# Kernel tuning notes

Measured on AMD Instinct MI355X. Metric: run time of the kernel, lower is better.

## Reference

```python
import jax, jax.numpy as jnp
import numpy as np

D_MODEL = 1024
HEADS = 16
DK = D_MODEL // HEADS
B, S = 2, 2048


def setup_inputs() -> dict:
    key = jax.random.key(0)
    ks = jax.random.split(key, 9)
    s = 0.02
    return {
        "Q": jax.random.normal(ks[0], (B, S, D_MODEL), jnp.float32),
        "K": jax.random.normal(ks[1], (B, S, D_MODEL), jnp.float32),
        "V": jax.random.normal(ks[2], (B, S, D_MODEL), jnp.float32),
        "mask": jnp.ones((B, 1, S), jnp.int32),
        "Wq": jax.random.normal(ks[3], (D_MODEL, D_MODEL), jnp.float32) * s,
        "Wk": jax.random.normal(ks[4], (D_MODEL, D_MODEL), jnp.float32) * s,
        "Wv": jax.random.normal(ks[5], (D_MODEL, D_MODEL), jnp.float32) * s,
        "Wo": jax.random.normal(ks[6], (D_MODEL, D_MODEL), jnp.float32) * s,
        "ln_gamma": jnp.ones((D_MODEL,), jnp.float32),
        "ln_beta": jnp.zeros((D_MODEL,), jnp.float32),
    }


def _layer_norm(x, gamma, beta, eps=1e-5):
    mu = jnp.mean(x, axis=-1, keepdims=True)
    var = jnp.mean(jnp.square(x - mu), axis=-1, keepdims=True)
    return (x - mu) * jax.lax.rsqrt(var + eps) * gamma + beta


def reference(Q, K, V, mask, Wq, Wk, Wv, Wo, ln_gamma, ln_beta):
    # torch Linear(no bias): y = x @ W.T
    def split_heads(x):  # [B,S,D] -> [B,H,S,dk]
        return x.reshape(B, -1, HEADS, DK).transpose(0, 2, 1, 3)

    q = split_heads(Q @ Wq.T)
    k = split_heads(K @ Wk.T)
    v = split_heads(V @ Wv.T)

    # scores: [B,H,Sq,Sk]
    scores = jnp.einsum("bhqd,bhkd->bhqk", q, k) / np.sqrt(DK).astype(np.float32)
    m = mask[:, None, :, :]  # [B,1,1,S] broadcast over heads and queries
    scores = jnp.where(m == 0, -jnp.inf, scores)
    attn = jax.nn.softmax(scores, axis=-1)  # dropout is identity in eval
    out = jnp.einsum("bhqk,bhkd->bhqd", attn, v)
    out = out.transpose(0, 2, 1, 3).reshape(B, -1, D_MODEL)
    out = out @ Wo.T
    return _layer_norm(out + Q, ln_gamma, ln_beta)
```

## Files before the change

kernel.cpp:

```cpp
#include <hip/hip_runtime.h>
#include <hip/hip_bf16.h>
#include <stdint.h>

#define NB 2
#define NS 2048
#define ND 1024
#define NH 16
#define NDK 64
#define NM (NB*NS)

using bf16x8 = __attribute__((ext_vector_type(8))) short;
using f32x4  = __attribute__((ext_vector_type(4))) float;
using f32x16 = __attribute__((ext_vector_type(16))) float;
using u32x4  = __attribute__((ext_vector_type(4))) unsigned;

__device__ __forceinline__ unsigned short f2bf(float f){
  unsigned u = __float_as_uint(f);
  u += 0x7fffu + ((u>>16)&1u);
  return (unsigned short)(u>>16);
}

__device__ __forceinline__ void gload_lds16(const void* g, void* l){
  __builtin_amdgcn_global_load_lds((const __attribute__((address_space(1))) void*)g,
                                   (__attribute__((address_space(3))) void*)l, 16, 0, 0);
}

__device__ __forceinline__ float fexp2(float x){
#if __has_builtin(__builtin_amdgcn_exp2f)
  return __builtin_amdgcn_exp2f(x);
#else
  return __expf(x * 0.69314718056f);
#endif
}

__device__ __forceinline__ unsigned cvtpk_bf16(float lo, float hi){
  unsigned r;
  asm("v_cvt_pk_bf16_f32 %0, %1, %2" : "=v"(r) : "v"(lo), "v"(hi));
  return r;
}

__device__ __forceinline__ void swap32(unsigned &a, unsigned &b){
#if __has_builtin(__builtin_amdgcn_permlane32_swap)
  auto rr = __builtin_amdgcn_permlane32_swap((int)a, (int)b, false, false);
  a = (unsigned)rr[0]; b = (unsigned)rr[1];
#else
  const bool lo = (threadIdx.x & 32) == 0;
  unsigned sa = (unsigned)__shfl_xor((int)a, 32, 64);
  unsigned sb = (unsigned)__shfl_xor((int)b, 32, 64);
  unsigned na = lo ? a : sb;
  unsigned nb = lo ? sa : b;
  a = na; b = nb;
#endif
}

__device__ __forceinline__ f32x16 mfma32(bf16x8 a, bf16x8 b, f32x16 c){
  return __builtin_amdgcn_mfma_f32_32x32x16_bf16(a, b, c, 0, 0, 0);
}

__global__ __launch_bounds__(256) void prep_k(const float* __restrict__ Q, const float* __restrict__ K,
                                              const float* __restrict__ V, const float* __restrict__ Wq,
                                              const float* __restrict__ Wk, const float* __restrict__ Wv,
                                              const float* __restrict__ Wo,
                                              unsigned short* __restrict__ Xbf,
                                              unsigned short* __restrict__ Wbf){
  const int bid = blockIdx.x;
  const float* src; unsigned short* dst; int i;
  if (bid < 12288){
    const int which = bid >> 12;
    src = (which==0) ? Q : (which==1) ? K : V;
    dst = Xbf + ((size_t)which << 22);
    i = (bid & 4095)*256 + threadIdx.x;
  } else {
    const int which = (bid - 12288) >> 10;
    src = (which==0) ? Wq : (which==1) ? Wk : (which==2) ? Wv : Wo;
    dst = Wbf + ((size_t)which << 20);
    i = ((bid - 12288) & 1023)*256 + threadIdx.x;
  }
  float4 v = ((const float4*)src)[i];
  ushort4 o;
  o.x = f2bf(v.x); o.y = f2bf(v.y); o.z = f2bf(v.z); o.w = f2bf(v.w);
  ((ushort4*)dst)[i] = o;
}

__global__ __launch_bounds__(256) void gemm_qkv(const short* __restrict__ Xbf, const short* __restrict__ Wbf,
                                                unsigned short* __restrict__ qh, unsigned short* __restrict__ kh,
                                                unsigned short* __restrict__ vT){
  __shared__ short lsA[2][4096];
  __shared__ short lsB[2][4096];
  const int tid = threadIdx.x;
  const int hw = blockIdx.x;
  const int logical = (hw & 7)*96 + (hw >> 3);
  const int z = logical >> 8, rem = logical & 255;
  const int my = rem >> 3, nx = rem & 7;
  const short* A = Xbf + (size_t)z*NM*ND;
  const short* W = Wbf + (size_t)z*ND*ND;
  unsigned short* out = (z==0) ? qh : (z==1) ? kh : vT;
  const int mode = (z==2) ? 1 : 0;
  const int m0 = my*128, n0 = nx*128;

  const short* gA = A + (size_t)m0*1024;
  const short* gB = W + (size_t)n0*1024;
  const int srow = tid>>2, scol = (tid&3)*8;
  const int w = tid>>6, lane = tid&63, lr = lane&15, lk = lane>>4;
  const int wm = w>>1, wn = w&1;

  f32x4 acc[4][4];
  #pragma unroll
  for (int i=0;i<4;++i)
    #pragma unroll
    for (int j=0;j<4;++j) acc[i][j] = (f32x4){0.f,0.f,0.f,0.f};

  #pragma unroll
  for (int r=0;r<2;++r){
    gload_lds16(gA + (size_t)(r*64+srow)*1024 + scol, &lsA[0][(r*256+tid)*8]);
    gload_lds16(gB + (size_t)(r*64+srow)*1024 + scol, &lsB[0][(r*256+tid)*8]);
  }
  int cur = 0;
  for (int ks=0; ks<32; ++ks){
    __syncthreads();
    if (ks+1 < 32){
      const int k0 = (ks+1)*32;
      #pragma unroll
      for (int r=0;r<2;++r){
        gload_lds16(gA + (size_t)(r*64+srow)*1024 + k0 + scol, &lsA[cur^1][(r*256+tid)*8]);
        gload_lds16(gB + (size_t)(r*64+srow)*1024 + k0 + scol, &lsB[cur^1][(r*256+tid)*8]);
      }
    }
    bf16x8 af[4], bfr[4];
    #pragma unroll
    for (int i=0;i<4;++i){
      af[i]  = *(const bf16x8*)&lsA[cur][(wm*64+i*16+lr)*32 + lk*8];
      bfr[i] = *(const bf16x8*)&lsB[cur][(wn*64+i*16+lr)*32 + lk*8];
    }
    #pragma unroll
    for (int i=0;i<4;++i)
      #pragma unroll
      for (int j=0;j<4;++j)
        acc[i][j] = __builtin_amdgcn_mfma_f32_16x16x32_bf16(af[i], bfr[j], acc[i][j], 0,0,0);
    cur ^= 1;
  }
  #pragma unroll
  for (int i=0;i<4;++i)
    #pragma unroll
    for (int j=0;j<4;++j)
      #pragma unroll
      for (int r=0;r<4;++r){
        const int m = m0 + wm*64 + i*16 + lk*4 + r;
        const int n = n0 + wn*64 + j*16 + lr;
        const float v = acc[i][j][r];
        const int b = m>>11, s = m&2047, h = n>>6, dk = n&63;
        size_t addr;
        if (mode == 0) addr = (((size_t)(b*NH+h))*NS + s)*NDK + dk;
        else           addr = (((size_t)(b*NH+h))*NDK + dk)*NS + s;
        out[addr] = f2bf(v);
      }
}

__global__ __launch_bounds__(256) void gemm_out(const short* __restrict__ Attn, const short* __restrict__ Wo,
                                                const float* __restrict__ Qin, float* __restrict__ proj){
  __shared__ short lsA[2][4096];
  __shared__ short lsB[2][4096];
  const int tid = threadIdx.x;
  const int hw = blockIdx.x;
  const int logical = (hw & 7)*32 + (hw >> 3);
  const int my = logical >> 3, nx = logical & 7;
  const int m0 = my*128, n0 = nx*128;
  const short* gA = Attn + (size_t)m0*1024;
  const short* gB = Wo + (size_t)n0*1024;
  const int srow = tid>>2, scol = (tid&3)*8;
  const int w = tid>>6, lane = tid&63, lr = lane&15, lk = lane>>4;
  const int wm = w>>1, wn = w&1;

  f32x4 acc[4][4];
  #pragma unroll
  for (int i=0;i<4;++i)
    #pragma unroll
    for (int j=0;j<4;++j) acc[i][j] = (f32x4){0.f,0.f,0.f,0.f};

  #pragma unroll
  for (int r=0;r<2;++r){
    gload_lds16(gA + (size_t)(r*64+srow)*1024 + scol, &lsA[0][(r*256+tid)*8]);
    gload_lds16(gB + (size_t)(r*64+srow)*1024 + scol, &lsB[0][(r*256+tid)*8]);
  }
  int cur = 0;
  for (int ks=0; ks<32; ++ks){
    __syncthreads();
    if (ks+1 < 32){
      const int k0 = (ks+1)*32;
      #pragma unroll
      for (int r=0;r<2;++r){
        gload_lds16(gA + (size_t)(r*64+srow)*1024 + k0 + scol, &lsA[cur^1][(r*256+tid)*8]);
        gload_lds16(gB + (size_t)(r*64+srow)*1024 + k0 + scol, &lsB[cur^1][(r*256+tid)*8]);
      }
    }
    bf16x8 af[4], bfr[4];
    #pragma unroll
    for (int i=0;i<4;++i){
      af[i]  = *(const bf16x8*)&lsA[cur][(wm*64+i*16+lr)*32 + lk*8];
      bfr[i] = *(const bf16x8*)&lsB[cur][(wn*64+i*16+lr)*32 + lk*8];
    }
    #pragma unroll
    for (int i=0;i<4;++i)
      #pragma unroll
      for (int j=0;j<4;++j)
        acc[i][j] = __builtin_amdgcn_mfma_f32_16x16x32_bf16(af[i], bfr[j], acc[i][j], 0,0,0);
    cur ^= 1;
  }
  #pragma unroll
  for (int i=0;i<4;++i)
    #pragma unroll
    for (int j=0;j<4;++j)
      #pragma unroll
      for (int r=0;r<4;++r){
        const int m = m0 + wm*64 + i*16 + lk*4 + r;
        const int n = n0 + wn*64 + j*16 + lr;
        proj[(size_t)m*1024 + n] = acc[i][j][r] + Qin[(size_t)m*1024 + n];
      }
}

__global__ __launch_bounds__(512) void attn_k(const short* __restrict__ qh, const short* __restrict__ kh,
                                              const short* __restrict__ vT, const int* __restrict__ mask,
                                              unsigned short* __restrict__ attn){
  __shared__ char sb[32768];
  const int bid = blockIdx.x;
  const int qb = bid & 7, h = (bid>>3)&15, b = bid>>7;
  const int tid = threadIdx.x, w = tid>>6, lane = tid&63;
  const int ql = lane & 31, hi = lane>>5;
  const int bh = b*NH + h;
  const int q0 = qb*256 + w*32;
  const float C2 = 0.18033688f;

  const int D = tid*16;
  const int strow = D>>7;
  const int S = D ^ ((strow&7)<<4);
  const char* ksrc  = (const char*)(kh + (size_t)bh*NS*NDK) + S;
  const char* vsrc  = (const char*)(vT + ((size_t)bh*NDK + strow)*NS) + (S & 127);

  const short* qrow = qh + ((size_t)bh*NS + q0 + ql)*NDK + hi*8;
  bf16x8 qf[4];
  #pragma unroll
  for (int kp=0;kp<4;++kp) qf[kp] = *(const bf16x8*)(qrow + kp*16);

  const int* mrow = mask + b*NS;

  f32x16 o0, o1;
  #pragma unroll
  for (int r=0;r<16;++r){ o0[r]=0.f; o1[r]=0.f; }
  float mrun = -1e30f, lrun = 0.f;

  const int swz = (ql&7)<<4;

  gload_lds16(ksrc, sb + D);
  gload_lds16(vsrc, sb + 16384 + D);

  for (int kt=0; kt<32; ++kt){
    const int kv0 = kt*64;
    const int buf = (kt&1)*8192;
    __syncthreads();
    if (kt+1 < 32){
      const int nbuf = ((kt+1)&1)*8192;
      gload_lds16(ksrc + (size_t)(kv0+64)*128, sb + nbuf + D);
      gload_lds16(vsrc + (size_t)(kv0+64)*2,   sb + 16384 + nbuf + D);
    }
    const unsigned long long bal = __ballot(mrow[kv0 + lane] != 0);
    const unsigned mw0 = (unsigned)bal, mw1 = (unsigned)(bal>>32);
    const bool allm = (~bal) == 0ull;

    bf16x8 kf[8];
    #pragma unroll
    for (int kvh=0;kvh<2;++kvh)
      #pragma unroll
      for (int kp=0;kp<4;++kp)
        kf[kvh*4+kp] = *(const bf16x8*)(sb + buf + (((kvh*32+ql)*128 + kp*32 + hi*16) ^ swz));

    f32x16 s0, s1;
    #pragma unroll
    for (int r=0;r<16;++r){ s0[r]=0.f; s1[r]=0.f; }
    #pragma unroll
    for (int kp=0;kp<4;++kp){
      s0 = mfma32(kf[kp],   qf[kp], s0);
      s1 = mfma32(kf[4+kp], qf[kp], s1);
    }

    float t[16];
    #pragma unroll
    for (int r=0;r<16;++r) t[r] = fmaxf(s0[r], s1[r]);
    #pragma unroll
    for (int st=8; st>=1; st>>=1)
      #pragma unroll
      for (int r=0;r<st;++r) t[r] = fmaxf(t[r], t[r+st]);
    const float tm = fmaxf(t[0], __shfl_xor(t[0], 32, 64));

    if (!__all(tm - mrun <= 32.f)){
      const float mnew = fmaxf(mrun, tm);
      const float fac  = fexp2((mrun - mnew)*C2);
      mrun = mnew;
      #pragma unroll
      for (int r=0;r<16;++r){ o0[r]*=fac; o1[r]*=fac; }
      lrun *= fac;
    }
    const float nb = mrun*C2;

    bf16x8 vf[8];
    #pragma unroll
    for (int dh=0;dh<2;++dh)
      #pragma unroll
      for (int c=0;c<4;++c)
        vf[dh*4+c] = *(const bf16x8*)(sb + 16384 + buf + (((dh*32+ql)*128 + c*32 + hi*16) ^ swz));

    float psum = 0.f;
    #pragma unroll
    for (int kvh=0; kvh<2; ++kvh){
      const f32x16& ss = kvh ? s1 : s0;
      const unsigned mw = kvh ? mw1 : mw0;
      unsigned pwd[8];
      float ps0 = 0.f, ps1 = 0.f;
      #pragma unroll
      for (int i=0;i<8;++i){
        const int bp0 = ((2*i)&3) + 8*((2*i)>>2);
        float p0 = fexp2(ss[2*i]*C2   - nb);
        float p1 = fexp2(ss[2*i+1]*C2 - nb);
        if (!allm){
          p0 = ((mw >> (bp0     + 4*hi)) & 1u) ? p0 : 0.f;
          p1 = ((mw >> (bp0 + 1 + 4*hi)) & 1u) ? p1 : 0.f;
        }
        ps0 += p0; ps1 += p1;
        pwd[i] = cvtpk_bf16(p0, p1);
      }
      psum += ps0 + ps1;
      swap32(pwd[0], pwd[2]);
      swap32(pwd[1], pwd[3]);
      swap32(pwd[4], pwd[6]);
      swap32(pwd[5], pwd[7]);
      u32x4 c0w = {pwd[0], pwd[1], pwd[2], pwd[3]};
      u32x4 c1w = {pwd[4], pwd[5], pwd[6], pwd[7]};
      bf16x8 pf0 = __builtin_bit_cast(bf16x8, c0w);
      bf16x8 pf1 = __builtin_bit_cast(bf16x8, c1w);
      o0 = mfma32(vf[0*4 + 2*kvh],     pf0, o0);
      o1 = mfma32(vf[1*4 + 2*kvh],     pf0, o1);
      o0 = mfma32(vf[0*4 + 2*kvh + 1], pf1, o0);
      o1 = mfma32(vf[1*4 + 2*kvh + 1], pf1, o1);
    }
    psum += __shfl_xor(psum, 32, 64);
    lrun += psum;
  }

  __syncthreads();
  const float inv = 1.f / lrun;
  char* ep = sb + w*4096;
  #pragma unroll
  for (int dh=0; dh<2; ++dh){
    const f32x16& oo = dh ? o1 : o0;
    #pragma unroll
    for (int i=0;i<8;++i){
      const int d0 = ((2*i)&3) + 8*((2*i)>>2) + 4*hi + dh*32;
      const unsigned pk = cvtpk_bf16(oo[2*i]*inv, oo[2*i+1]*inv);
      *(unsigned*)(ep + (((ql*128) + d0*2) ^ ((ql&7)<<4))) = pk;
    }
  }
  asm volatile("s_waitcnt lgkmcnt(0)" ::: "memory");
  #pragma unroll
  for (int seg=0; seg<4; ++seg){
    const int qq = seg*8 + (lane>>3), dc = (lane&7)*8;
    bf16x8 vv = *(const bf16x8*)(ep + (((qq*128) + dc*2) ^ ((qq&7)<<4)));
    *(bf16x8*)(attn + ((size_t)b*NS + q0 + qq)*ND + h*NDK + dc) = vv;
  }
}

__global__ __launch_bounds__(256) void ln_k(const float* __restrict__ proj,
                                            const float* __restrict__ gamma, const float* __restrict__ beta,
                                            float* __restrict__ out){
  const int row = blockIdx.x*4 + (threadIdx.x>>6);
  const int lane = threadIdx.x & 63;
  const float4* pp = (const float4*)(proj + (size_t)row*ND);
  float4 x[4];
  float sum = 0.f;
  #pragma unroll
  for (int i=0;i<4;++i){
    x[i] = pp[lane + i*64];
    sum += x[i].x + x[i].y + x[i].z + x[i].w;
  }
  #pragma unroll
  for (int off=32; off>=1; off>>=1) sum += __shfl_xor(sum, off, 64);
  const float mu = sum * (1.f/1024.f);
  float vs = 0.f;
  #pragma unroll
  for (int i=0;i<4;++i){
    float d0=x[i].x-mu, d1=x[i].y-mu, d2=x[i].z-mu, d3=x[i].w-mu;
    vs += d0*d0 + d1*d1 + d2*d2 + d3*d3;
  }
  #pragma unroll
  for (int off=32; off>=1; off>>=1) vs += __shfl_xor(vs, off, 64);
  const float rstd = rsqrtf(vs*(1.f/1024.f) + 1e-5f);
  #pragma unroll
  for (int i=0;i<4;++i){
    const float4 g  = ((const float4*)gamma)[lane + i*64];
    const float4 be = ((const float4*)beta)[lane + i*64];
    float4 y;
    y.x = (x[i].x-mu)*rstd*g.x + be.x;
    y.y = (x[i].y-mu)*rstd*g.y + be.y;
    y.z = (x[i].z-mu)*rstd*g.z + be.z;
    y.w = (x[i].w-mu)*rstd*g.w + be.w;
    ((float4*)(out + (size_t)row*ND))[lane + i*64] = y;
  }
}

extern "C" void kernel_launch(void* const* d_in, const int* in_sizes, int n_in,
                              void* d_out, int out_size, void* d_ws, size_t ws_size,
                              hipStream_t stream){
  const float* Q    = (const float*)d_in[0];
  const float* K    = (const float*)d_in[1];
  const float* V    = (const float*)d_in[2];
  const int*   mask = (const int*)  d_in[3];
  const float* Wq   = (const float*)d_in[4];
  const float* Wk   = (const float*)d_in[5];
  const float* Wv   = (const float*)d_in[6];
  const float* Wo   = (const float*)d_in[7];
  const float* gam  = (const float*)d_in[8];
  const float* bet  = (const float*)d_in[9];
  float* out = (float*)d_out;
  char* ws = (char*)d_ws;

  unsigned short* Wbf  = (unsigned short*)(ws);
  unsigned short* Xbf  = (unsigned short*)(ws + (size_t)(8u<<20));
  unsigned short* qhp  = (unsigned short*)(ws + (size_t)(32u<<20));
  unsigned short* khp  = (unsigned short*)(ws + (size_t)(40u<<20));
  unsigned short* vTp  = (unsigned short*)(ws + (size_t)(48u<<20));
  unsigned short* attb = (unsigned short*)(ws + (size_t)(56u<<20));
  float* proj  = (float*)(ws + (size_t)(8u<<20));

  prep_k<<<16384,256,0,stream>>>(Q, K, V, Wq, Wk, Wv, Wo, Xbf, Wbf);

  gemm_qkv<<<768,256,0,stream>>>((const short*)Xbf, (const short*)Wbf, qhp, khp, vTp);

  attn_k<<<256,512,0,stream>>>((const short*)qhp, (const short*)khp, (const short*)vTp, mask, attb);

  gemm_out<<<256,256,0,stream>>>((const short*)attb, (const short*)(Wbf + (3u<<20)), Q, proj);

  ln_k<<<1024,256,0,stream>>>(proj, gam, bet, out);
}
```

Measured before the change: 161.1 us.

## Split attention KV range across two wave groups and merge partial softmax states

Attention blocks now cover 128 queries instead of 256 and the grid doubles to 512. Within a block the eight waves form two halves that each process half of the KV sequence, and their running max, sum and output accumulators are combined through LDS at the end. The mask ballots are also precomputed once into LDS. This is meant to fill the GPU's compute units better, since 256 blocks underfill the device, at the cost of twice the K/V LDS traffic per query, more LDS use (about 66KB) and an extra reduction step.

```diff
diff --git a/kernel.cpp b/kernel.cpp
--- a/kernel.cpp
+++ b/kernel.cpp
@@ -221,20 +221,21 @@
 __global__ __launch_bounds__(512) void attn_k(const short* __restrict__ qh, const short* __restrict__ kh,
                                               const short* __restrict__ vT, const int* __restrict__ mask,
                                               unsigned short* __restrict__ attn){
-  __shared__ char sb[32768];
+  __shared__ char sb[66048];
   const int bid = blockIdx.x;
-  const int qb = bid & 7, h = (bid>>3)&15, b = bid>>7;
+  const int qb = bid & 15, h = (bid>>4)&15, b = bid>>8;
   const int tid = threadIdx.x, w = tid>>6, lane = tid&63;
   const int ql = lane & 31, hi = lane>>5;
+  const int qw = w & 3, half = w>>2;
   const int bh = b*NH + h;
-  const int q0 = qb*256 + w*32;
+  const int q0 = qb*128 + qw*32;
   const float C2 = 0.18033688f;
 
   const int D = tid*16;
   const int strow = D>>7;
   const int S = D ^ ((strow&7)<<4);
-  const char* ksrc  = (const char*)(kh + (size_t)bh*NS*NDK) + S;
-  const char* vsrc  = (const char*)(vT + ((size_t)bh*NDK + strow)*NS) + (S & 127);
+  const char* ksrc = (const char*)(kh + (size_t)bh*NS*NDK) + S;
+  const char* vsrc = (const char*)(vT + ((size_t)bh*NDK + strow)*NS) + (S & 127);
 
   const short* qrow = qh + ((size_t)bh*NS + q0 + ql)*NDK + hi*8;
   bf16x8 qf[4];
@@ -242,6 +243,19 @@
   for (int kp=0;kp<4;++kp) qf[kp] = *(const bf16x8*)(qrow + kp*16);
 
   const int* mrow = mask + b*NS;
+  unsigned long long* smask = (unsigned long long*)(sb + 65536);
+
+  gload_lds16(ksrc,                      sb + D);
+  gload_lds16(ksrc + (size_t)1024*128,   sb + 8192 + D);
+  gload_lds16(vsrc,                      sb + 32768 + D);
+  gload_lds16(vsrc + (size_t)1024*2,     sb + 32768 + 8192 + D);
+
+  #pragma unroll
+  for (int j=0;j<4;++j){
+    const int gt = w*4 + j;
+    const unsigned long long bal = __ballot(mrow[gt*64 + lane] != 0);
+    if (lane == 0) smask[gt] = bal;
+  }
 
   f32x16 o0, o1;
   #pragma unroll
@@ -250,28 +264,30 @@
 
   const int swz = (ql&7)<<4;
 
-  gload_lds16(ksrc, sb + D);
-  gload_lds16(vsrc, sb + 16384 + D);
-
-  for (int kt=0; kt<32; ++kt){
-    const int kv0 = kt*64;
-    const int buf = (kt&1)*8192;
+  for (int t=0; t<16; ++t){
+    const int buf = (t&1)*16384;
     __syncthreads();
-    if (kt+1 < 32){
-      const int nbuf = ((kt+1)&1)*8192;
-      gload_lds16(ksrc + (size_t)(kv0+64)*128, sb + nbuf + D);
-      gload_lds16(vsrc + (size_t)(kv0+64)*2,   sb + 16384 + nbuf + D);
-    }
-    const unsigned long long bal = __ballot(mrow[kv0 + lane] != 0);
-    const unsigned mw0 = (unsigned)bal, mw1 = (unsigned)(bal>>32);
-    const bool allm = (~bal) == 0ull;
+    if (t+1 < 16){
+      const int nbuf = ((t+1)&1)*16384;
+      const size_t kvn0 = (size_t)(t+1)*64, kvn1 = 1024 + kvn0;
+      gload_lds16(ksrc + kvn0*128, sb + nbuf + D);
+      gload_lds16(ksrc + kvn1*128, sb + nbuf + 8192 + D);
+      gload_lds16(vsrc + kvn0*2,   sb + 32768 + nbuf + D);
+      gload_lds16(vsrc + kvn1*2,   sb + 32768 + nbuf + 8192 + D);
+    }
+    const unsigned long long m64 = smask[half*16 + t];
+    const unsigned mw0 = (unsigned)m64, mw1 = (unsigned)(m64>>32);
+    const bool allm = (~m64) == 0ull;
+
+    const char* kb = sb + buf + half*8192;
+    const char* vb = sb + 32768 + buf + half*8192;
 
     bf16x8 kf[8];
     #pragma unroll
     for (int kvh=0;kvh<2;++kvh)
       #pragma unroll
       for (int kp=0;kp<4;++kp)
-        kf[kvh*4+kp] = *(const bf16x8*)(sb + buf + (((kvh*32+ql)*128 + kp*32 + hi*16) ^ swz));
+        kf[kvh*4+kp] = *(const bf16x8*)(kb + (((kvh*32+ql)*128 + kp*32 + hi*16) ^ swz));
 
     f32x16 s0, s1;
     #pragma unroll
@@ -282,14 +298,14 @@
       s1 = mfma32(kf[4+kp], qf[kp], s1);
     }
 
-    float t[16];
-    #pragma unroll
-    for (int r=0;r<16;++r) t[r] = fmaxf(s0[r], s1[r]);
+    float t16[16];
+    #pragma unroll
+    for (int r=0;r<16;++r) t16[r] = fmaxf(s0[r], s1[r]);
     #pragma unroll
     for (int st=8; st>=1; st>>=1)
       #pragma unroll
-      for (int r=0;r<st;++r) t[r] = fmaxf(t[r], t[r+st]);
-    const float tm = fmaxf(t[0], __shfl_xor(t[0], 32, 64));
+      for (int r=0;r<st;++r) t16[r] = fmaxf(t16[r], t16[r+st]);
+    const float tm = fmaxf(t16[0], __shfl_xor(t16[0], 32, 64));
 
     if (!__all(tm - mrun <= 32.f)){
       const float mnew = fmaxf(mrun, tm);
@@ -306,7 +322,7 @@
     for (int dh=0;dh<2;++dh)
       #pragma unroll
       for (int c=0;c<4;++c)
-        vf[dh*4+c] = *(const bf16x8*)(sb + 16384 + buf + (((dh*32+ql)*128 + c*32 + hi*16) ^ swz));
+        vf[dh*4+c] = *(const bf16x8*)(vb + (((dh*32+ql)*128 + c*32 + hi*16) ^ swz));
 
     float psum = 0.f;
     #pragma unroll
@@ -336,34 +352,61 @@
       u32x4 c1w = {pwd[4], pwd[5], pwd[6], pwd[7]};
       bf16x8 pf0 = __builtin_bit_cast(bf16x8, c0w);
       bf16x8 pf1 = __builtin_bit_cast(bf16x8, c1w);
-      o0 = mfma32(vf[0*4 + 2*kvh],     pf0, o0);
-      o1 = mfma32(vf[1*4 + 2*kvh],     pf0, o1);
-      o0 = mfma32(vf[0*4 + 2*kvh + 1], pf1, o0);
-      o1 = mfma32(vf[1*4 + 2*kvh + 1], pf1, o1);
+      o0 = mfma32(vf[2*kvh],       pf0, o0);
+      o1 = mfma32(vf[4 + 2*kvh],   pf0, o1);
+      o0 = mfma32(vf[2*kvh + 1],   pf1, o0);
+      o1 = mfma32(vf[4 + 2*kvh+1], pf1, o1);
     }
     psum += __shfl_xor(psum, 32, 64);
     lrun += psum;
   }
 
   __syncthreads();
-  const float inv = 1.f / lrun;
-  char* ep = sb + w*4096;
-  #pragma unroll
-  for (int dh=0; dh<2; ++dh){
-    const f32x16& oo = dh ? o1 : o0;
-    #pragma unroll
-    for (int i=0;i<8;++i){
-      const int d0 = ((2*i)&3) + 8*((2*i)>>2) + 4*hi + dh*32;
-      const unsigned pk = cvtpk_bf16(oo[2*i]*inv, oo[2*i+1]*inv);
-      *(unsigned*)(ep + (((ql*128) + d0*2) ^ ((ql&7)<<4))) = pk;
-    }
-  }
-  asm volatile("s_waitcnt lgkmcnt(0)" ::: "memory");
-  #pragma unroll
-  for (int seg=0; seg<4; ++seg){
-    const int qq = seg*8 + (lane>>3), dc = (lane&7)*8;
-    bf16x8 vv = *(const bf16x8*)(ep + (((qq*128) + dc*2) ^ ((qq&7)<<4)));
-    *(bf16x8*)(attn + ((size_t)b*NS + q0 + qq)*ND + h*NDK + dc) = vv;
+  float* smm = (float*)(sb + 32768);
+  float* sml = (float*)(sb + 32768 + 1024);
+  if (hi == 0){ smm[w*32 + ql] = mrun; sml[w*32 + ql] = lrun; }
+  __syncthreads();
+  const float pmv = smm[(w^4)*32 + ql], plv = sml[(w^4)*32 + ql];
+  const float mfin = fmaxf(mrun, pmv);
+  const float facS = fexp2((mrun - mfin)*C2);
+  if (w >= 4){
+    float* eg = (float*)(sb + (size_t)(w-4)*8192);
+    #pragma unroll
+    for (int r=0;r<16;++r){
+      eg[ql + 32*(hi*16 + r)]        = o0[r]*facS;
+      eg[ql + 32*(hi*16 + r) + 1024] = o1[r]*facS;
+    }
+  }
+  __syncthreads();
+  if (w < 4){
+    float* eg = (float*)(sb + (size_t)w*8192);
+    #pragma unroll
+    for (int r=0;r<16;++r){
+      o0[r] = o0[r]*facS + eg[ql + 32*(hi*16 + r)];
+      o1[r] = o1[r]*facS + eg[ql + 32*(hi*16 + r) + 1024];
+    }
+    const float facP = fexp2((pmv - mfin)*C2);
+    const float lfin = lrun*facS + plv*facP;
+    const float inv = 1.f / lfin;
+    asm volatile("s_waitcnt lgkmcnt(0)" ::: "memory");
+    char* ep = sb + (size_t)w*8192;
+    #pragma unroll
+    for (int dh=0; dh<2; ++dh){
+      const f32x16& oo = dh ? o1 : o0;
+      #pragma unroll
+      for (int i=0;i<8;++i){
+        const int d0 = ((2*i)&3) + 8*((2*i)>>2) + 4*hi + dh*32;
+        const unsigned pk = cvtpk_bf16(oo[2*i]*inv, oo[2*i+1]*inv);
+        *(unsigned*)(ep + (((ql*128) + d0*2) ^ ((ql&7)<<4))) = pk;
+      }
+    }
+    asm volatile("s_waitcnt lgkmcnt(0)" ::: "memory");
+    #pragma unroll
+    for (int seg=0; seg<4; ++seg){
+      const int qq = seg*8 + (lane>>3), dc = (lane&7)*8;
+      bf16x8 vv = *(const bf16x8*)(ep + (((qq*128) + dc*2) ^ ((qq&7)<<4)));
+      *(bf16x8*)(attn + ((size_t)b*NS + q0 + qq)*ND + h*NDK + dc) = vv;
+    }
   }
 }
 
@@ -433,7 +476,7 @@
 
   gemm_qkv<<<768,256,0,stream>>>((const short*)Xbf, (const short*)Wbf, qhp, khp, vTp);
 
-  attn_k<<<256,512,0,stream>>>((const short*)qhp, (const short*)khp, (const short*)vTp, mask, attb);
+  attn_k<<<512,512,0,stream>>>((const short*)qhp, (const short*)khp, (const short*)vTp, mask, attb);
 
   gemm_out<<<256,256,0,stream>>>((const short*)attb, (const short*)(Wbf + (3u<<20)), Q, proj);
 
```

Measured after the change: 173.2 us. 1.08x slower.
